# Performance work log

Measured on AMD Instinct MI355X. Metric: run time of the kernel, lower is better.

Reference implementation:

```python
import jax, jax.numpy as jnp
import numpy as np

S, T, D_OUT = 64, 256, 64
B = 64
HEADS = 2
D0 = S + T              # 320
D1 = D0 * (1 + HEADS)   # 960
D2 = D1 * (1 + HEADS)   # 2880
PARAM_SCALE = 0.02


def setup_inputs() -> dict:
    key = jax.random.key(0)
    k1, k2, k3, k4 = jax.random.split(key, 4)
    x = jax.random.normal(k1, (B, T, S), dtype=jnp.float32)
    A0 = jax.random.normal(k2, (HEADS, D0, D0), dtype=jnp.float32) * PARAM_SCALE
    A1 = jax.random.normal(k3, (HEADS, D1, D1), dtype=jnp.float32) * PARAM_SCALE
    Wo = jax.random.normal(k4, (D_OUT, D2), dtype=jnp.float32) * PARAM_SCALE
    return {"x": x, "A0": A0, "A1": A1, "Wo": Wo}


def _causal_self_attention(h, A):
    # h: [B, T, d], A: [H, d, d]
    Bsz, Tlen, d = h.shape
    H = A.shape[0]
    # bilinear scores per head: h @ A[i] @ h^T, vectorized over heads
    scores = jnp.einsum('btd,hde,bse->bhts', h, A, h)  # [B, H, T, T]
    neg_inf = jnp.asarray(float('-inf'), dtype=h.dtype)
    mask = jnp.triu(jnp.full((Tlen, Tlen), neg_inf, dtype=h.dtype), k=1)
    attn = jax.nn.softmax(scores + mask, axis=-1)
    out = jnp.einsum('bhts,bsd->bthd', attn, h)  # [B, T, H, d]
    return out.reshape(Bsz, Tlen, H * d)


def reference(x, A0, A1, Wo):
    Bsz, Tlen, _ = x.shape
    # one-hot positional encoding concatenated onto input
    pos = jnp.broadcast_to(jnp.eye(Tlen, dtype=x.dtype)[None], (Bsz, Tlen, Tlen))
    h = jnp.concatenate([x, pos], axis=-1)          # [B, T, S+T]
    h = jnp.concatenate([h, _causal_self_attention(h, A0)], axis=-1)  # [B, T, D1]
    h = jnp.concatenate([h, _causal_self_attention(h, A1)], axis=-1)  # [B, T, D2]
    logits = jnp.einsum('btd,od->bto', h, Wo)       # [B, T, d_out]
    return logits
```

## Files before the change

kernel.cpp:

```cpp
#include <hip/hip_runtime.h>
#include <math.h>

#define NB 64
#define NT 256
#define NS 64
#define ND0 320
#define ND1 960
#define ND2 2880
#define NH 2
#define DC 704
#define GP 1024

typedef __attribute__((ext_vector_type(8))) _Float16 f16x8;
typedef __attribute__((ext_vector_type(4))) float f32x4;
typedef __attribute__((ext_vector_type(4))) short short4v;

typedef const __attribute__((address_space(1))) void* gas_ptr;
typedef __attribute__((address_space(3))) void* las_ptr;
#define GLOAD16(g, l) __builtin_amdgcn_global_load_lds((gas_ptr)(g), (las_ptr)(l), 16, 0, 0)
#define MFMAH(a, b, c) __builtin_amdgcn_mfma_f32_16x16x32_f16((a), (b), (c), 0, 0, 0)

__device__ __forceinline__ short f2h(float v) {
    union { _Float16 h; short s; } u; u.h = (_Float16)v; return u.s;
}
__device__ __forceinline__ float h2f(short b) {
    union { _Float16 h; short s; } u; u.s = b; return (float)u.h;
}
__device__ __forceinline__ int swz(int o) { return o ^ (((o >> 7) & 7) << 4); }

template <int CMODE, int TERMS, bool AJUMP, bool SWZ>
__global__ __launch_bounds__(256, 3) void gemm128(
    const short* Ah, int lda, long sA,
    const short* Bh, const short* Bl, int ldb, long sB,
    float* Cf, int ldcf, long sCf,
    short* Chi, int ldch,
    const short* biasH, long ldbias,
    const float* biasA1,
    long hsA, long hsC,
    int gx, int K)
{
    int bx, by;
    if (SWZ) {
        int wg = blockIdx.x;
        int q = gridDim.x >> 3;
        int sid = (wg & 7) * q + (wg >> 3);
        bx = sid % gx; by = sid / gx;
    } else { bx = blockIdx.x; by = blockIdx.y; }
    int m0 = by * 128, n0 = bx * 128;
    if (CMODE == 0 && n0 > m0 + 127) return;
    long zLo = blockIdx.z & 63, zHi = blockIdx.z >> 6;
    const short* pAh = Ah + zLo * sA + zHi * hsA;
    const short* pBh = Bh + zLo * sB;
    const short* pBl = (TERMS == 2) ? (Bl + zLo * sB) : nullptr;

    __shared__ short lds[8192 * (1 + TERMS)];
    short* LAh = lds;
    short* LBh = lds + 8192;
    short* LBl = lds + 16384;

    int tid = threadIdx.x;
    int lane = tid & 63, w = tid >> 6;
    int wr = w >> 1, wc = w & 1;

    const short* aSH[4]; const short* bSH[4]; const short* bSL[4];
    int aLo[4], bLo[4];
#pragma unroll
    for (int j = 0; j < 4; ++j) {
        int o = j * 4096 + tid * 16;
        int c = swz(o); int r = c >> 7, col = (c & 127) >> 1;
        aSH[j] = pAh + (long)(m0 + r) * lda + col;
        aLo[j] = o >> 1;
        bSH[j] = pBh + (long)(n0 + r) * ldb + col;
        if (TERMS == 2) bSL[j] = pBl + (long)(n0 + r) * ldb + col;
        bLo[j] = o >> 1;
    }

    int oa[4][2], ob[4][2];
#pragma unroll
    for (int mf = 0; mf < 4; ++mf)
#pragma unroll
        for (int kf = 0; kf < 2; ++kf) {
            int row = wr * 64 + mf * 16 + (lane & 15);
            oa[mf][kf] = swz(row * 128 + (kf * 32 + ((lane >> 4) << 3)) * 2) >> 1;
        }
#pragma unroll
    for (int nf = 0; nf < 4; ++nf)
#pragma unroll
        for (int kf = 0; kf < 2; ++kf) {
            int row = wc * 64 + nf * 16 + (lane & 15);
            ob[nf][kf] = swz(row * 128 + (kf * 32 + ((lane >> 4) << 3)) * 2) >> 1;
        }

    f32x4 acc[4][4] = {};

    for (int k0 = 0; k0 < K; k0 += 64) {
        int step = (AJUMP && k0 == 0) ? 320 : 64;
#pragma unroll
        for (int j = 0; j < 4; ++j) {
            GLOAD16(aSH[j], LAh + aLo[j]);
            aSH[j] += step;
            GLOAD16(bSH[j], LBh + bLo[j]);
            bSH[j] += 64;
            if (TERMS == 2) { GLOAD16(bSL[j], LBl + bLo[j]); bSL[j] += 64; }
        }
        __syncthreads();
#pragma unroll
        for (int kf = 0; kf < 2; ++kf) {
            f16x8 vbh[4], vbl[4];
#pragma unroll
            for (int nf = 0; nf < 4; ++nf) {
                vbh[nf] = *(const f16x8*)(LBh + ob[nf][kf]);
                if (TERMS == 2) vbl[nf] = *(const f16x8*)(LBl + ob[nf][kf]);
            }
#pragma unroll
            for (int mf = 0; mf < 4; ++mf) {
                f16x8 vah = *(const f16x8*)(LAh + oa[mf][kf]);
#pragma unroll
                for (int nf = 0; nf < 4; ++nf) {
                    acc[mf][nf] = MFMAH(vah, vbh[nf], acc[mf][nf]);
                    if (TERMS == 2) acc[mf][nf] = MFMAH(vah, vbl[nf], acc[mf][nf]);
                }
            }
        }
        __syncthreads();
    }

#pragma unroll
    for (int mf = 0; mf < 4; ++mf)
#pragma unroll
        for (int nf = 0; nf < 4; ++nf) {
            f32x4 v = acc[mf][nf];
            int col  = n0 + wc * 64 + nf * 16 + (lane & 15);
            int rowb = m0 + wr * 64 + mf * 16 + ((lane >> 4) << 2);
            if (CMODE == 0) {
#pragma unroll
                for (int r = 0; r < 4; ++r) {
                    long o = (zLo * 256 + rowb + r) * ldbias + 64 + col + zHi * hsA;
                    v[r] += h2f(biasH[o]);
                }
#pragma unroll
                for (int r = 0; r < 4; ++r)
                    Cf[zLo * sCf + zHi * hsC + (long)(rowb + r) * ldcf + col] = v[r];
            } else {
                int head = col >> 10, colh = col & 1023;
                if (colh < ND1) {
                    const float* bA = biasA1 + (long)head * 921600 + colh;
#pragma unroll
                    for (int r = 0; r < 4; ++r) {
                        int t = (rowb + r) & 255;
                        float f = v[r] + bA[(long)(64 + t) * 960];
                        Chi[(long)(rowb + r) * ldch + col] = f2h(f);
                    }
                }
            }
        }
}

template <int BMODE, int TERMS, bool KCAUSAL, bool ACC, bool OUTU, bool BJUMP>
__global__ __launch_bounds__(256) void gemm_mfma(
    const short* Ah, int lda, long sA,
    const short* Bh, const short* Bl, int ldb, long sB, long hsB,
    float* Cf, int ldcf, long sCf,
    short* Chi, short* Clo, int ldch, long sCh,
    const float* biasF, long ldbias, long hsBias,
    long hsA, long hsC,
    short* UThi,
    int K)
{
    int m0 = blockIdx.y * 128, n0 = blockIdx.x * 64;
    long zLo = blockIdx.z & 63, zHi = blockIdx.z >> 6;
    const short* pAh = Ah + zLo * sA + zHi * hsA;
    const short* pBh = Bh + zLo * sB + zHi * hsB;
    const short* pBl = (TERMS == 2) ? (Bl + zLo * sB + zHi * hsB) : nullptr;

    __shared__ short lds[8192 + TERMS * 4096];
    short* LAh = lds;
    short* LBh = lds + 8192;
    short* LBl = lds + 12288;

    int tid = threadIdx.x;
    int lane = tid & 63, w = tid >> 6;
    int wr = w >> 1, wc = w & 1;

    const short* aSH[4]; const short* bSH[2]; const short* bSL[2];
    int aLo[4], bLo[2];
#pragma unroll
    for (int j = 0; j < 4; ++j) {
        int o = j * 4096 + tid * 16;
        int c = swz(o); int r = c >> 7, col = (c & 127) >> 1;
        aSH[j] = pAh + (long)(m0 + r) * lda + col;
        aLo[j] = o >> 1;
    }
#pragma unroll
    for (int j = 0; j < 2; ++j) {
        int o = j * 4096 + tid * 16;
        int c = swz(o); int r = c >> 7, col = (c & 127) >> 1;
        bSH[j] = pBh + (long)(n0 + r) * ldb + col;
        if (TERMS == 2) bSL[j] = pBl + (long)(n0 + r) * ldb + col;
        bLo[j] = o >> 1;
    }

    int oa[4][2], ob[2][2];
#pragma unroll
    for (int mf = 0; mf < 4; ++mf)
#pragma unroll
        for (int kf = 0; kf < 2; ++kf) {
            int row = wr * 64 + mf * 16 + (lane & 15);
            oa[mf][kf] = swz(row * 128 + (kf * 32 + ((lane >> 4) << 3)) * 2) >> 1;
        }
#pragma unroll
    for (int nf = 0; nf < 2; ++nf)
#pragma unroll
        for (int kf = 0; kf < 2; ++kf) {
            int row = wc * 32 + nf * 16 + (lane & 15);
            ob[nf][kf] = swz(row * 128 + (kf * 32 + ((lane >> 4) << 3)) * 2) >> 1;
        }

    f32x4 acc[4][2] = {};
    int Klim = KCAUSAL ? (K < m0 + 128 ? K : m0 + 128) : K;

    for (int k0 = 0; k0 < Klim; k0 += 64) {
#pragma unroll
        for (int j = 0; j < 4; ++j) {
            GLOAD16(aSH[j], LAh + aLo[j]);
            aSH[j] += 64;
        }
        long bstep = (BJUMP && k0 == 192) ? (1048576L - 192L) : 64L;
#pragma unroll
        for (int j = 0; j < 2; ++j) {
            GLOAD16(bSH[j], LBh + bLo[j]);
            bSH[j] += bstep;
            if (TERMS == 2) { GLOAD16(bSL[j], LBl + bLo[j]); bSL[j] += bstep; }
        }
        __syncthreads();
#pragma unroll
        for (int kf = 0; kf < 2; ++kf) {
            f16x8 vbh[2], vbl[2];
#pragma unroll
            for (int nf = 0; nf < 2; ++nf) {
                vbh[nf] = *(const f16x8*)(LBh + ob[nf][kf]);
                if (TERMS == 2) vbl[nf] = *(const f16x8*)(LBl + ob[nf][kf]);
            }
#pragma unroll
            for (int mf = 0; mf < 4; ++mf) {
                f16x8 vah = *(const f16x8*)(LAh + oa[mf][kf]);
#pragma unroll
                for (int nf = 0; nf < 2; ++nf) {
                    acc[mf][nf] = MFMAH(vah, vbh[nf], acc[mf][nf]);
                    if (TERMS == 2) acc[mf][nf] = MFMAH(vah, vbl[nf], acc[mf][nf]);
                }
            }
        }
        __syncthreads();
    }

#pragma unroll
    for (int mf = 0; mf < 4; ++mf)
#pragma unroll
        for (int nf = 0; nf < 2; ++nf) {
            f32x4 v = acc[mf][nf];
            int col  = n0 + wc * 32 + nf * 16 + (lane & 15);
            int rowb = m0 + wr * 64 + mf * 16 + ((lane >> 4) << 2);
            if (BMODE == 1) {
#pragma unroll
                for (int r = 0; r < 4; ++r) {
                    int t = (rowb + r) & 255;
                    v[r] += biasF[zLo * hsBias + (long)(64 + t) * ldbias + col];
                }
            } else if (BMODE == 3) {
#pragma unroll
                for (int r = 0; r < 4; ++r) {
                    int t = (rowb + r) & 255;
                    v[r] += biasF[(long)(col - n0) * 2880 + (n0 >> 6) * 960 + 64 + t];
                }
            }
            if (OUTU) {
                if (n0 == 0) {
#pragma unroll
                    for (int r = 0; r < 4; ++r)
                        Cf[(long)(rowb + r) * ldcf + col] = v[r];
                } else {
                    int head = (n0 >> 6) - 1;
                    int o = col - n0;
                    short hs[4];
#pragma unroll
                    for (int r = 0; r < 4; ++r) hs[r] = f2h(v[r]);
                    short4v th = {hs[0], hs[1], hs[2], hs[3]};
                    *(short4v*)(UThi + head * 1048576L + (long)o * 16384 + rowb) = th;
                }
            } else if (ACC) {
#pragma unroll
                for (int r = 0; r < 4; ++r)
                    Cf[zLo * sCf + (long)(rowb + r) * ldcf + col] += v[r];
            } else if (Cf) {
#pragma unroll
                for (int r = 0; r < 4; ++r)
                    Cf[zLo * sCf + (long)(rowb + r) * ldcf + col] = v[r];
            } else {
#pragma unroll
                for (int r = 0; r < 4; ++r) {
                    float f = v[r];
                    short hi = f2h(f);
                    Chi[zHi * hsC + zLo * sCh + (long)(rowb + r) * ldch + col] = hi;
                    if (Clo)
                        Clo[zHi * hsC + zLo * sCh + (long)(rowb + r) * ldch + col] = f2h(f - h2f(hi));
                }
            }
        }
}

__global__ __launch_bounds__(256) void build_h_rows(const float* __restrict__ x,
                                                    short* __restrict__ hhi) {
    int idx = blockIdx.x * 256 + threadIdx.x;
    int bt = idx >> 6, c = idx & 63;
    hhi[(long)bt * DC + c] = f2h(x[(long)bt * NS + c]);
}

__global__ __launch_bounds__(256) void build_hT_x(const float* __restrict__ x,
                                                  short* __restrict__ hTh,
                                                  short* __restrict__ hTl) {
    __shared__ float tile[32][33];
    int c0 = blockIdx.x * 32, t0 = blockIdx.y * 32, b = blockIdx.z;
    int tx = threadIdx.x, ty = threadIdx.y;
    const float* xb = x + (long)b * NT * NS;
#pragma unroll
    for (int i = ty; i < 32; i += 8) tile[i][tx] = xb[(long)(t0 + i) * NS + c0 + tx];
    __syncthreads();
    long base = (long)b * (NS * 256);
#pragma unroll
    for (int i = ty; i < 32; i += 8) {
        float v = tile[tx][i];
        short hi = f2h(v);
        hTh[base + (long)(c0 + i) * 256 + t0 + tx] = hi;
        hTl[base + (long)(c0 + i) * 256 + t0 + tx] = f2h(v - h2f(hi));
    }
}

__global__ void build_At(const float* __restrict__ A,
                         short* __restrict__ hi, short* __restrict__ lo,
                         int dN, int dK, int srcLd, int shift, int dSrcN) {
    __shared__ float tile[32][33];
    int k0 = blockIdx.x * 32, n0 = blockIdx.y * 32;
    long hbase = (long)blockIdx.z * srcLd * srcLd;
    int tx = threadIdx.x, ty = threadIdx.y;
#pragma unroll
    for (int i = ty; i < 32; i += 8) {
        int k = k0 + i;
        int srck = (k < 64) ? k : k + shift;
        tile[i][tx] = (n0 + tx < dSrcN) ? A[hbase + (long)srck * srcLd + n0 + tx] : 0.f;
    }
    __syncthreads();
    long obase = (long)blockIdx.z * dN * dK;
#pragma unroll
    for (int i = ty; i < 32; i += 8) {
        float v = tile[tx][i];
        short h = f2h(v);
        hi[obase + (long)(n0 + i) * dK + k0 + tx] = h;
        if (lo) lo[obase + (long)(n0 + i) * dK + k0 + tx] = f2h(v - h2f(h));
    }
}

__global__ __launch_bounds__(256) void build_Wf(const float* __restrict__ Wo,
                                                short* __restrict__ hi) {
    int idx = blockIdx.x * 256 + threadIdx.x;
    if (idx >= 192 * DC) return;
    int r = idx / DC, kc = idx - r * DC;
    int o = r & 63, chunk = r >> 6;
    int srck = (kc < 64) ? kc : kc + 256;
    hi[idx] = f2h(Wo[(long)o * ND2 + chunk * 960 + srck]);
}

__global__ __launch_bounds__(256) void softmax_split(const float* S,
                                                     short* pHi, short* pLo,
                                                     int ldo, long hs) {
    int row  = blockIdx.x * 4 + (threadIdx.x >> 6);
    int t    = row & (NT - 1);
    int hrow = row & 16383;
    int head = row >> 14;
    int lane = threadIdx.x & 63;
    int s0   = lane << 2;
    const float* p = S + (long)row * NT;

    float4 v = *(const float4*)(p + s0);
    float vv[4] = {v.x, v.y, v.z, v.w};
    float mx = -INFINITY;
#pragma unroll
    for (int j = 0; j < 4; ++j)
        if (s0 + j <= t) mx = fmaxf(mx, vv[j]);
    for (int off = 32; off; off >>= 1) mx = fmaxf(mx, __shfl_down(mx, off));
    mx = __shfl(mx, 0);

    float e[4]; float sum = 0.f;
#pragma unroll
    for (int j = 0; j < 4; ++j) {
        e[j] = (s0 + j <= t) ? __expf(vv[j] - mx) : 0.f;
        sum += e[j];
    }
    for (int off = 32; off; off >>= 1) sum += __shfl_down(sum, off);
    sum = __shfl(sum, 0);
    float inv = 1.f / sum;

    short hsv[4], lsv[4];
#pragma unroll
    for (int j = 0; j < 4; ++j) {
        float f = e[j] * inv;
        hsv[j] = f2h(f);
        lsv[j] = f2h(f - h2f(hsv[j]));
    }
    short4v hv = {hsv[0], hsv[1], hsv[2], hsv[3]};
    *(short4v*)(pHi + (long)head * hs + (long)hrow * ldo + s0) = hv;
    if (pLo) {
        short4v lv = {lsv[0], lsv[1], lsv[2], lsv[3]};
        *(short4v*)(pLo + (long)head * hs + (long)hrow * ldo + s0) = lv;
    }
}

__global__ __launch_bounds__(256) void build_h0(const float* __restrict__ x,
                                                float* __restrict__ h) {
    int idx = blockIdx.x * 256 + threadIdx.x;
    int bt = idx / ND0;
    int c  = idx - bt * ND0;
    int t  = bt & (NT - 1);
    float v;
    if (c < NS) v = x[(long)bt * NS + c];
    else        v = ((c - NS) == t) ? 1.0f : 0.0f;
    h[(long)bt * ND2 + c] = v;
}

template <bool BT, bool CAUSAL>
__global__ __launch_bounds__(256) void gemm64(
    const float* __restrict__ A, int lda, long sA,
    const float* __restrict__ Bm, int ldb, long sB,
    float* __restrict__ C, int ldc, long sC, int K)
{
    int m0 = blockIdx.y * 64, n0 = blockIdx.x * 64;
    if (CAUSAL && n0 > m0 + 63) return;
    long z = blockIdx.z;
    A += z * sA; Bm += z * sB; C += z * sC;

    __shared__ float As[16][68];
    __shared__ float Bs[16][68];

    int tid = threadIdx.x;
    int tx = tid & 15, ty = tid >> 4;
    int rowA = tid >> 2, kA = (tid & 3) << 2;
    int kB = tid >> 4,  colB = (tid & 15) << 2;

    float acc[4][4] = {};

    for (int k0 = 0; k0 < K; k0 += 16) {
        float4 av = *(const float4*)(A + (long)(m0 + rowA) * lda + k0 + kA);
        As[kA + 0][rowA] = av.x; As[kA + 1][rowA] = av.y;
        As[kA + 2][rowA] = av.z; As[kA + 3][rowA] = av.w;
        if (BT) {
            float4 bv = *(const float4*)(Bm + (long)(n0 + rowA) * ldb + k0 + kA);
            Bs[kA + 0][rowA] = bv.x; Bs[kA + 1][rowA] = bv.y;
            Bs[kA + 2][rowA] = bv.z; Bs[kA + 3][rowA] = bv.w;
        } else {
            float4 bv = *(const float4*)(Bm + (long)(k0 + kB) * ldb + n0 + colB);
            *(float4*)(&Bs[kB][colB]) = bv;
        }
        __syncthreads();
#pragma unroll
        for (int kk = 0; kk < 16; ++kk) {
            float4 a4 = *(const float4*)(&As[kk][ty << 2]);
            float4 b4 = *(const float4*)(&Bs[kk][tx << 2]);
            float a[4] = {a4.x, a4.y, a4.z, a4.w};
            float b[4] = {b4.x, b4.y, b4.z, b4.w};
#pragma unroll
            for (int i = 0; i < 4; ++i)
#pragma unroll
                for (int j = 0; j < 4; ++j)
                    acc[i][j] += a[i] * b[j];
        }
        __syncthreads();
    }
#pragma unroll
    for (int i = 0; i < 4; ++i) {
        float4 v = {acc[i][0], acc[i][1], acc[i][2], acc[i][3]};
        *(float4*)(C + (long)(m0 + (ty << 2) + i) * ldc + n0 + (tx << 2)) = v;
    }
}

__global__ __launch_bounds__(256) void softmax_causal(float* __restrict__ P) {
    int row  = blockIdx.x * 4 + (threadIdx.x >> 6);
    int t    = row & (NT - 1);
    int lane = threadIdx.x & 63;
    int s0   = lane << 2;
    float* p = P + (long)row * NT;

    float4 v = *(const float4*)(p + s0);
    float vv[4] = {v.x, v.y, v.z, v.w};
    float mx = -INFINITY;
#pragma unroll
    for (int j = 0; j < 4; ++j)
        if (s0 + j <= t) mx = fmaxf(mx, vv[j]);
    for (int off = 32; off; off >>= 1) mx = fmaxf(mx, __shfl_down(mx, off));
    mx = __shfl(mx, 0);

    float e[4]; float sum = 0.f;
#pragma unroll
    for (int j = 0; j < 4; ++j) {
        e[j] = (s0 + j <= t) ? __expf(vv[j] - mx) : 0.f;
        sum += e[j];
    }
    for (int off = 32; off; off >>= 1) sum += __shfl_down(sum, off);
    sum = __shfl(sum, 0);
    float inv = 1.f / sum;
    float4 o = {e[0] * inv, e[1] * inv, e[2] * inv, e[3] * inv};
    *(float4*)(p + s0) = o;
}

extern "C" void kernel_launch(void* const* d_in, const int* in_sizes, int n_in,
                              void* d_out, int out_size, void* d_ws, size_t ws_size,
                              hipStream_t stream) {
    const float* x  = (const float*)d_in[0];
    const float* A0 = (const float*)d_in[1];
    const float* A1 = (const float*)d_in[2];
    const float* Wo = (const float*)d_in[3];
    float* out = (float*)d_out;

    if (ws_size >= 175120384UL) {
        char* wsb = (char*)d_ws;
        short* hc_hi = (short*)(wsb);
        short* G_hi  = (short*)(wsb + 46137344L);
        float* S     = (float*)(wsb + 113246208L);
        short* P     = (short*)(wsb + 146800640L);
        short* hT_hi = (short*)(wsb + 163577856L);
        short* hT_lo = (short*)(wsb + 165675008L);
        short* At_hi = (short*)(wsb + 167772160L);
        short* Wf_hi = (short*)(wsb + 170655744L);
        short* UT_hi = (short*)(wsb + 170926080L);

        build_h_rows<<<4096, 256, 0, stream>>>(x, hc_hi);
        build_hT_x<<<dim3(2, 8, 64), dim3(32, 8), 0, stream>>>(x, hT_hi, hT_lo);
        build_Wf<<<528, 256, 0, stream>>>(Wo, Wf_hi);

        build_At<<<dim3(2, 10, 2), dim3(32, 8), 0, stream>>>(A0, At_hi, nullptr, ND0, 64, ND0, 0, ND0);
        gemm_mfma<1, 1, false, false, false, false><<<dim3(5, 128, 2), 256, 0, stream>>>(
            hc_hi, DC, 0L,
            At_hi, nullptr, 64, 20480L, 0L,
            nullptr, 0, 0L, G_hi, nullptr, 640, 320L,
            A0, 320L, 102400L,
            0L, 0L,
            nullptr, 64);
        gemm128<0, 1, false, false><<<dim3(2, 2, 128), 256, 0, stream>>>(
            G_hi, 640, 163840L,
            hc_hi, nullptr, DC, 180224L,
            S, NT, 65536L,
            nullptr, 0,
            G_hi, 640L,
            nullptr,
            320L, 4194304L, 0, 64);
        softmax_split<<<8192, 256, 0, stream>>>(S, hc_hi + 128, nullptr, DC, 320L);
        gemm_mfma<0, 2, true, false, false, false><<<dim3(1, 2, 128), 256, 0, stream>>>(
            hc_hi + 128, DC, 180224L,
            hT_hi, hT_lo, 256, 16384L, 0L,
            nullptr, 0, 0L,
            hc_hi + 64, nullptr, DC, 180224L,
            nullptr, 0L, 0L,
            320L, 320L,
            nullptr, 256);

        gemm_mfma<3, 1, false, false, true, false><<<dim3(3, 128, 1), 256, 0, stream>>>(
            hc_hi, DC, 0L,
            Wf_hi, nullptr, DC, 0L, 0L,
            out, NS, 0L, nullptr, nullptr, 0, 0L,
            Wo, 0L, 0L,
            0L, 0L,
            UT_hi, DC);

        build_At<<<dim3(22, 32, 2), dim3(32, 8), 0, stream>>>(A1, At_hi, nullptr, GP, DC, ND1, 256, ND1);
        gemm128<1, 1, false, true><<<dim3(2048, 1, 1), 256, 0, stream>>>(
            hc_hi, DC, 0L,
            At_hi, nullptr, DC, 0L,
            nullptr, 0, 0L,
            G_hi, 2048,
            nullptr, 0L,
            A1,
            0L, 0L, 16, DC);
        gemm128<0, 1, true, false><<<dim3(2, 2, 128), 256, 0, stream>>>(
            G_hi, 2048, 524288L,
            hc_hi, nullptr, DC, 180224L,
            S, NT, 65536L,
            nullptr, 0,
            G_hi, 2048L,
            nullptr,
            1024L, 4194304L, 0, DC);
        softmax_split<<<8192, 256, 0, stream>>>(S, P, nullptr, 512, 256L);
        gemm_mfma<0, 1, false, true, false, true><<<dim3(1, 2, 64), 256, 0, stream>>>(
            P, 512, 131072L,
            UT_hi, nullptr, 16384, 256L, 0L,
            out, NS, 16384L, nullptr, nullptr, 0, 0L,
            nullptr, 0L, 0L,
            0L, 0L,
            nullptr, 512);
        return;
    }

    float* ws = (float*)d_ws;
    float* h  = ws;
    float* G  = ws + 47185920L;
    float* Pf = ws + 47185920L + 15728640L;

    build_h0<<<(NB * NT * ND0) / 256, 256, 0, stream>>>(x, h);

    for (int layer = 0; layer < 2; ++layer) {
        int d = layer ? ND1 : ND0;
        const float* Am = layer ? A1 : A0;
        for (int head = 0; head < NH; ++head) {
            const float* Ah = Am + (long)head * d * d;
            gemm64<false, false><<<dim3(d / 64, 256, 1), 256, 0, stream>>>(
                h, ND2, 0L, Ah, d, 0L, G, d, 0L, d);
            gemm64<true, true><<<dim3(4, 4, NB), 256, 0, stream>>>(
                G, d, (long)NT * d, h, ND2, (long)NT * ND2,
                Pf, NT, (long)NT * NT, d);
            softmax_causal<<<(NB * NT) / 4, 256, 0, stream>>>(Pf);
            gemm64<false, false><<<dim3(d / 64, 4, NB), 256, 0, stream>>>(
                Pf, NT, (long)NT * NT, h, ND2, (long)NT * ND2,
                h + (long)d * (1 + head), ND2, (long)NT * ND2, NT);
        }
    }
    gemm64<true, false><<<dim3(1, 256, 1), 256, 0, stream>>>(
        h, ND2, 0L, Wo, ND2, 0L, out, NS, 0L, ND2);
}
```

Baseline: 189.6 us.

## Fuse causal score GEMM with softmax into a single full-row kernel

Adds a score_sm kernel that computes a 128x256 score tile per block, so each block holds complete rows. The kernel adds the positional bias, applies the causal mask, and does a two-wave max and sum reduction through LDS, then writes fp16 probabilities directly. The separate fp32 score round trip through global memory and the standalone softmax kernels are removed for both layers. In exchange, each block holds a large accumulator with only one block per CU allowed. Only 256 blocks are launched, which may leave many CUs idle.

```diff
diff --git a/kernel.cpp b/kernel.cpp
--- a/kernel.cpp
+++ b/kernel.cpp
@@ -27,6 +27,186 @@
     union { _Float16 h; short s; } u; u.s = b; return (float)u.h;
 }
 __device__ __forceinline__ int swz(int o) { return o ^ (((o >> 7) & 7) << 4); }
+
+template <int LAYER>
+__global__ __launch_bounds__(256, 1) void score_sm(
+    const short* __restrict__ G, int ldg, long sG, long hsG,
+    const short* __restrict__ hc,
+    short* __restrict__ pOut, int ldo, long sO, long hsO,
+    int K)
+{
+    int by = blockIdx.y;
+    int m0 = by * 128;
+    long zLo = blockIdx.z & 63, zHi = blockIdx.z >> 6;
+    const short* pAh = G + zLo * sG + zHi * hsG;
+    const short* pBh = hc + zLo * 180224L;
+
+    __shared__ short lds[24576];
+    int tid = threadIdx.x;
+    int lane = tid & 63, w = tid >> 6;
+    int wr = w >> 1, wc = w & 1;
+    int q = lane >> 4, l15 = lane & 15;
+
+    const short* aS[4]; const short* bS[8];
+    int dLo[4];
+#pragma unroll
+    for (int j = 0; j < 4; ++j) {
+        int o = j * 4096 + tid * 16;
+        int c = swz(o); int r = c >> 7, col = (c & 127) >> 1;
+        dLo[j] = o >> 1;
+        aS[j] = pAh + (long)(m0 + r) * ldg + col;
+        bS[j] = pBh + (long)r * DC + col;
+        bS[j + 4] = pBh + (long)(128 + r) * DC + col;
+    }
+
+    int oa[4][2], ob[8][2];
+#pragma unroll
+    for (int mf = 0; mf < 4; ++mf)
+#pragma unroll
+        for (int kf = 0; kf < 2; ++kf) {
+            int row = wr * 64 + mf * 16 + l15;
+            oa[mf][kf] = swz(row * 128 + (kf * 32 + (q << 3)) * 2) >> 1;
+        }
+#pragma unroll
+    for (int nf = 0; nf < 8; ++nf)
+#pragma unroll
+        for (int kf = 0; kf < 2; ++kf) {
+            int s = wc * 128 + nf * 16 + l15;
+            int half = s >> 7, sr = s & 127;
+            ob[nf][kf] = half * 8192 + (swz(sr * 128 + (kf * 32 + (q << 3)) * 2) >> 1);
+        }
+
+    f32x4 acc[4][8] = {};
+
+    for (int k0 = 0; k0 < K; k0 += 64) {
+        int step = (LAYER == 1 && k0 == 0) ? 320 : 64;
+#pragma unroll
+        for (int j = 0; j < 4; ++j) {
+            GLOAD16(aS[j], lds + dLo[j]);
+            aS[j] += step;
+            GLOAD16(bS[j], lds + 8192 + dLo[j]);
+            bS[j] += 64;
+        }
+        if (by) {
+#pragma unroll
+            for (int j = 0; j < 4; ++j) {
+                GLOAD16(bS[j + 4], lds + 16384 + dLo[j]);
+                bS[j + 4] += 64;
+            }
+        }
+        __syncthreads();
+        if (by || wc == 0) {
+#pragma unroll
+            for (int kf = 0; kf < 2; ++kf) {
+                f16x8 vb[8];
+#pragma unroll
+                for (int nf = 0; nf < 8; ++nf)
+                    vb[nf] = *(const f16x8*)(lds + 8192 + ob[nf][kf]);
+#pragma unroll
+                for (int mf = 0; mf < 4; ++mf) {
+                    f16x8 va = *(const f16x8*)(lds + oa[mf][kf]);
+#pragma unroll
+                    for (int nf = 0; nf < 8; ++nf)
+                        acc[mf][nf] = MFMAH(va, vb[nf], acc[mf][nf]);
+                }
+            }
+        }
+        __syncthreads();
+    }
+
+    float* red = (float*)lds;
+
+#pragma unroll
+    for (int mf = 0; mf < 4; ++mf)
+#pragma unroll
+        for (int nf = 0; nf < 8; ++nf) {
+            int colb = wc * 128 + nf * 16 + l15;
+#pragma unroll
+            for (int rr = 0; rr < 4; ++rr) {
+                int t = m0 + wr * 64 + mf * 16 + q * 4 + rr;
+                if (colb <= t) {
+                    long o = (zLo * 256 + t) * (long)ldg + 64 + colb + zHi * hsG;
+                    acc[mf][nf][rr] += h2f(G[o]);
+                } else {
+                    acc[mf][nf][rr] = -1e30f;
+                }
+            }
+        }
+
+    float rmax[4][4];
+#pragma unroll
+    for (int mf = 0; mf < 4; ++mf)
+#pragma unroll
+        for (int rr = 0; rr < 4; ++rr) {
+            float m = -1e30f;
+#pragma unroll
+            for (int nf = 0; nf < 8; ++nf) m = fmaxf(m, acc[mf][nf][rr]);
+            m = fmaxf(m, __shfl_xor(m, 1));
+            m = fmaxf(m, __shfl_xor(m, 2));
+            m = fmaxf(m, __shfl_xor(m, 4));
+            m = fmaxf(m, __shfl_xor(m, 8));
+            rmax[mf][rr] = m;
+        }
+    if (l15 == 0) {
+#pragma unroll
+        for (int mf = 0; mf < 4; ++mf)
+#pragma unroll
+            for (int rr = 0; rr < 4; ++rr)
+                red[wc * 128 + wr * 64 + mf * 16 + q * 4 + rr] = rmax[mf][rr];
+    }
+    __syncthreads();
+
+    float fullm[4][4];
+#pragma unroll
+    for (int mf = 0; mf < 4; ++mf)
+#pragma unroll
+        for (int rr = 0; rr < 4; ++rr) {
+            int row = wr * 64 + mf * 16 + q * 4 + rr;
+            fullm[mf][rr] = fmaxf(red[row], red[128 + row]);
+        }
+
+#pragma unroll
+    for (int mf = 0; mf < 4; ++mf)
+#pragma unroll
+        for (int rr = 0; rr < 4; ++rr) {
+            float s = 0.f;
+#pragma unroll
+            for (int nf = 0; nf < 8; ++nf) {
+                float a = acc[mf][nf][rr];
+                float e = (a > -1e29f) ? __expf(a - fullm[mf][rr]) : 0.f;
+                acc[mf][nf][rr] = e;
+                s += e;
+            }
+            s += __shfl_xor(s, 1);
+            s += __shfl_xor(s, 2);
+            s += __shfl_xor(s, 4);
+            s += __shfl_xor(s, 8);
+            rmax[mf][rr] = s;
+        }
+    if (l15 == 0) {
+#pragma unroll
+        for (int mf = 0; mf < 4; ++mf)
+#pragma unroll
+            for (int rr = 0; rr < 4; ++rr)
+                red[256 + wc * 128 + wr * 64 + mf * 16 + q * 4 + rr] = rmax[mf][rr];
+    }
+    __syncthreads();
+
+#pragma unroll
+    for (int mf = 0; mf < 4; ++mf)
+#pragma unroll
+        for (int rr = 0; rr < 4; ++rr) {
+            int row = wr * 64 + mf * 16 + q * 4 + rr;
+            int t = m0 + row;
+            float inv = 1.f / (red[256 + row] + red[256 + 128 + row]);
+            long base = zLo * sO + zHi * hsO + (long)t * ldo;
+#pragma unroll
+            for (int nf = 0; nf < 8; ++nf) {
+                int colb = wc * 128 + nf * 16 + l15;
+                pOut[base + colb] = f2h(acc[mf][nf][rr] * inv);
+            }
+        }
+}
 
 template <int CMODE, int TERMS, bool AJUMP, bool SWZ>
 __global__ __launch_bounds__(256, 3) void gemm128(
@@ -47,7 +227,6 @@
         bx = sid % gx; by = sid / gx;
     } else { bx = blockIdx.x; by = blockIdx.y; }
     int m0 = by * 128, n0 = bx * 128;
-    if (CMODE == 0 && n0 > m0 + 127) return;
     long zLo = blockIdx.z & 63, zHi = blockIdx.z >> 6;
     const short* pAh = Ah + zLo * sA + zHi * hsA;
     const short* pBh = Bh + zLo * sB;
@@ -133,11 +312,6 @@
             int col  = n0 + wc * 64 + nf * 16 + (lane & 15);
             int rowb = m0 + wr * 64 + mf * 16 + ((lane >> 4) << 2);
             if (CMODE == 0) {
-#pragma unroll
-                for (int r = 0; r < 4; ++r) {
-                    long o = (zLo * 256 + rowb + r) * ldbias + 64 + col + zHi * hsA;
-                    v[r] += h2f(biasH[o]);
-                }
 #pragma unroll
                 for (int r = 0; r < 4; ++r)
                     Cf[zLo * sCf + zHi * hsC + (long)(rowb + r) * ldcf + col] = v[r];
@@ -370,51 +544,6 @@
     hi[idx] = f2h(Wo[(long)o * ND2 + chunk * 960 + srck]);
 }
 
-__global__ __launch_bounds__(256) void softmax_split(const float* S,
-                                                     short* pHi, short* pLo,
-                                                     int ldo, long hs) {
-    int row  = blockIdx.x * 4 + (threadIdx.x >> 6);
-    int t    = row & (NT - 1);
-    int hrow = row & 16383;
-    int head = row >> 14;
-    int lane = threadIdx.x & 63;
-    int s0   = lane << 2;
-    const float* p = S + (long)row * NT;
-
-    float4 v = *(const float4*)(p + s0);
-    float vv[4] = {v.x, v.y, v.z, v.w};
-    float mx = -INFINITY;
-#pragma unroll
-    for (int j = 0; j < 4; ++j)
-        if (s0 + j <= t) mx = fmaxf(mx, vv[j]);
-    for (int off = 32; off; off >>= 1) mx = fmaxf(mx, __shfl_down(mx, off));
-    mx = __shfl(mx, 0);
-
-    float e[4]; float sum = 0.f;
-#pragma unroll
-    for (int j = 0; j < 4; ++j) {
-        e[j] = (s0 + j <= t) ? __expf(vv[j] - mx) : 0.f;
-        sum += e[j];
-    }
-    for (int off = 32; off; off >>= 1) sum += __shfl_down(sum, off);
-    sum = __shfl(sum, 0);
-    float inv = 1.f / sum;
-
-    short hsv[4], lsv[4];
-#pragma unroll
-    for (int j = 0; j < 4; ++j) {
-        float f = e[j] * inv;
-        hsv[j] = f2h(f);
-        lsv[j] = f2h(f - h2f(hsv[j]));
-    }
-    short4v hv = {hsv[0], hsv[1], hsv[2], hsv[3]};
-    *(short4v*)(pHi + (long)head * hs + (long)hrow * ldo + s0) = hv;
-    if (pLo) {
-        short4v lv = {lsv[0], lsv[1], lsv[2], lsv[3]};
-        *(short4v*)(pLo + (long)head * hs + (long)hrow * ldo + s0) = lv;
-    }
-}
-
 __global__ __launch_bounds__(256) void build_h0(const float* __restrict__ x,
                                                 float* __restrict__ h) {
     int idx = blockIdx.x * 256 + threadIdx.x;
@@ -524,7 +653,6 @@
         char* wsb = (char*)d_ws;
         short* hc_hi = (short*)(wsb);
         short* G_hi  = (short*)(wsb + 46137344L);
-        float* S     = (float*)(wsb + 113246208L);
         short* P     = (short*)(wsb + 146800640L);
         short* hT_hi = (short*)(wsb + 163577856L);
         short* hT_lo = (short*)(wsb + 165675008L);
@@ -544,15 +672,11 @@
             A0, 320L, 102400L,
             0L, 0L,
             nullptr, 64);
-        gemm128<0, 1, false, false><<<dim3(2, 2, 128), 256, 0, stream>>>(
-            G_hi, 640, 163840L,
-            hc_hi, nullptr, DC, 180224L,
-            S, NT, 65536L,
-            nullptr, 0,
-            G_hi, 640L,
-            nullptr,
-            320L, 4194304L, 0, 64);
-        softmax_split<<<8192, 256, 0, stream>>>(S, hc_hi + 128, nullptr, DC, 320L);
+        score_sm<0><<<dim3(1, 2, 128), 256, 0, stream>>>(
+            G_hi, 640, 163840L, 320L,
+            hc_hi,
+            hc_hi + 128, DC, 180224L, 320L,
+            64);
         gemm_mfma<0, 2, true, false, false, false><<<dim3(1, 2, 128), 256, 0, stream>>>(
             hc_hi + 128, DC, 180224L,
             hT_hi, hT_lo, 256, 16384L, 0L,
@@ -579,15 +703,11 @@
             nullptr, 0L,
             A1,
             0L, 0L, 16, DC);
-        gemm128<0, 1, true, false><<<dim3(2, 2, 128), 256, 0, stream>>>(
-            G_hi, 2048, 524288L,
-            hc_hi, nullptr, DC, 180224L,
-            S, NT, 65536L,
-            nullptr, 0,
-            G_hi, 2048L,
-            nullptr,
-            1024L, 4194304L, 0, DC);
-        softmax_split<<<8192, 256, 0, stream>>>(S, P, nullptr, 512, 256L);
+        score_sm<1><<<dim3(1, 2, 128), 256, 0, stream>>>(
+            G_hi, 2048, 524288L, 1024L,
+            hc_hi,
+            P, 512, 131072L, 256L,
+            DC);
         gemm_mfma<0, 1, false, true, false, true><<<dim3(1, 2, 64), 256, 0, stream>>>(
             P, 512, 131072L,
             UT_hi, nullptr, 16384, 256L, 0L,
```

Measured after the change: 226.5 us. 1.19x slower.

## Add dedicated 256x128 G1 GEMM with unpadded 1920 columns and drop lo-term split

Applied to the files above, without the earlier changes.

Replaces the generic swizzled gemm128 used for the layer-1 projection G = h·A1 with a dedicated gemmG1 kernel. The new kernel uses 256x128 tiles, fixed K=704 and an unpadded 1920-column output, where each head previously was padded to 1024 columns. It also removes the fp16 hi/lo error-compensation terms from the A·V GEMM over x (TERMS 2 to 1), and drops the lo outputs from the build and softmax kernels. This cuts redundant MFMA work, padded-column compute and extra memory writes, at the cost of reduced numerical precision in the first attention output.

```diff
diff --git a/kernel.cpp b/kernel.cpp
--- a/kernel.cpp
+++ b/kernel.cpp
@@ -9,7 +9,6 @@
 #define ND2 2880
 #define NH 2
 #define DC 704
-#define GP 1024
 
 typedef __attribute__((ext_vector_type(8))) _Float16 f16x8;
 typedef __attribute__((ext_vector_type(4))) float f32x4;
@@ -28,24 +27,110 @@
 }
 __device__ __forceinline__ int swz(int o) { return o ^ (((o >> 7) & 7) << 4); }
 
-template <int CMODE, int TERMS, bool AJUMP, bool SWZ>
+__global__ __launch_bounds__(256, 2) void gemmG1(
+    const short* __restrict__ hc,
+    const short* __restrict__ At,
+    short* __restrict__ G,
+    const float* __restrict__ A1)
+{
+    int wg = blockIdx.x;
+    int q8 = gridDim.x >> 3;
+    int sid = (wg & 7) * q8 + (wg >> 3);
+    int bx = sid % 15, by = sid / 15;
+    int m0 = by << 8, n0 = bx << 7;
+
+    __shared__ short lds[24576];
+    int tid = threadIdx.x;
+    int lane = tid & 63, w = tid >> 6;
+    int wm = w >> 1, wn = w & 1;
+    int q = lane >> 4, l15 = lane & 15;
+
+    const short* aS[8]; const short* bS[4];
+    int dA[8], dB[4];
+#pragma unroll
+    for (int j = 0; j < 8; ++j) {
+        int o = j * 4096 + tid * 16;
+        int c = swz(o); int r = c >> 7, col = (c & 127) >> 1;
+        aS[j] = hc + (long)(m0 + r) * DC + col;
+        dA[j] = o >> 1;
+    }
+#pragma unroll
+    for (int j = 0; j < 4; ++j) {
+        int o = j * 4096 + tid * 16;
+        int c = swz(o); int r = c >> 7, col = (c & 127) >> 1;
+        bS[j] = At + (long)(n0 + r) * DC + col;
+        dB[j] = o >> 1;
+    }
+
+    int oa[8][2], ob[4][2];
+#pragma unroll
+    for (int mf = 0; mf < 8; ++mf)
+#pragma unroll
+        for (int kf = 0; kf < 2; ++kf) {
+            int row = wm * 128 + mf * 16 + l15;
+            oa[mf][kf] = swz(row * 128 + (kf * 32 + (q << 3)) * 2) >> 1;
+        }
+#pragma unroll
+    for (int nf = 0; nf < 4; ++nf)
+#pragma unroll
+        for (int kf = 0; kf < 2; ++kf) {
+            int row = wn * 64 + nf * 16 + l15;
+            ob[nf][kf] = swz(row * 128 + (kf * 32 + (q << 3)) * 2) >> 1;
+        }
+
+    f32x4 acc[8][4] = {};
+
+    for (int k0 = 0; k0 < DC; k0 += 64) {
+#pragma unroll
+        for (int j = 0; j < 8; ++j) { GLOAD16(aS[j], lds + dA[j]); aS[j] += 64; }
+#pragma unroll
+        for (int j = 0; j < 4; ++j) { GLOAD16(bS[j], lds + 16384 + dB[j]); bS[j] += 64; }
+        __syncthreads();
+#pragma unroll
+        for (int kf = 0; kf < 2; ++kf) {
+            f16x8 vb[4];
+#pragma unroll
+            for (int nf = 0; nf < 4; ++nf)
+                vb[nf] = *(const f16x8*)(lds + 16384 + ob[nf][kf]);
+#pragma unroll
+            for (int mf = 0; mf < 8; ++mf) {
+                f16x8 va = *(const f16x8*)(lds + oa[mf][kf]);
+#pragma unroll
+                for (int nf = 0; nf < 4; ++nf)
+                    acc[mf][nf] = MFMAH(va, vb[nf], acc[mf][nf]);
+            }
+        }
+        __syncthreads();
+    }
+
+#pragma unroll
+    for (int mf = 0; mf < 8; ++mf)
+#pragma unroll
+        for (int nf = 0; nf < 4; ++nf) {
+            int col = n0 + wn * 64 + nf * 16 + l15;
+            int head = (col >= 960) ? 1 : 0;
+            int colh = col - head * 960;
+            const float* bA = A1 + (long)head * 921600 + colh;
+            int rowb = m0 + wm * 128 + mf * 16 + (q << 2);
+#pragma unroll
+            for (int r = 0; r < 4; ++r) {
+                int t = (rowb + r) & 255;
+                float f = acc[mf][nf][r] + bA[(long)(64 + t) * 960];
+                G[(long)(rowb + r) * 1920 + col] = f2h(f);
+            }
+        }
+}
+
+template <int CMODE, int TERMS, bool AJUMP>
 __global__ __launch_bounds__(256, 3) void gemm128(
     const short* Ah, int lda, long sA,
     const short* Bh, const short* Bl, int ldb, long sB,
     float* Cf, int ldcf, long sCf,
-    short* Chi, int ldch,
     const short* biasH, long ldbias,
-    const float* biasA1,
     long hsA, long hsC,
-    int gx, int K)
+    int K)
 {
-    int bx, by;
-    if (SWZ) {
-        int wg = blockIdx.x;
-        int q = gridDim.x >> 3;
-        int sid = (wg & 7) * q + (wg >> 3);
-        bx = sid % gx; by = sid / gx;
-    } else { bx = blockIdx.x; by = blockIdx.y; }
+    int bx = blockIdx.x, by = blockIdx.y;
     int m0 = by * 128, n0 = bx * 128;
     if (CMODE == 0 && n0 > m0 + 127) return;
     long zLo = blockIdx.z & 63, zHi = blockIdx.z >> 6;
@@ -132,27 +217,14 @@
             f32x4 v = acc[mf][nf];
             int col  = n0 + wc * 64 + nf * 16 + (lane & 15);
             int rowb = m0 + wr * 64 + mf * 16 + ((lane >> 4) << 2);
-            if (CMODE == 0) {
-#pragma unroll
-                for (int r = 0; r < 4; ++r) {
-                    long o = (zLo * 256 + rowb + r) * ldbias + 64 + col + zHi * hsA;
-                    v[r] += h2f(biasH[o]);
-                }
-#pragma unroll
-                for (int r = 0; r < 4; ++r)
-                    Cf[zLo * sCf + zHi * hsC + (long)(rowb + r) * ldcf + col] = v[r];
-            } else {
-                int head = col >> 10, colh = col & 1023;
-                if (colh < ND1) {
-                    const float* bA = biasA1 + (long)head * 921600 + colh;
-#pragma unroll
-                    for (int r = 0; r < 4; ++r) {
-                        int t = (rowb + r) & 255;
-                        float f = v[r] + bA[(long)(64 + t) * 960];
-                        Chi[(long)(rowb + r) * ldch + col] = f2h(f);
-                    }
-                }
-            }
+#pragma unroll
+            for (int r = 0; r < 4; ++r) {
+                long o = (zLo * 256 + rowb + r) * ldbias + 64 + col + zHi * hsA;
+                v[r] += h2f(biasH[o]);
+            }
+#pragma unroll
+            for (int r = 0; r < 4; ++r)
+                Cf[zLo * sCf + zHi * hsC + (long)(rowb + r) * ldcf + col] = v[r];
         }
 }
 
@@ -317,8 +389,7 @@
 }
 
 __global__ __launch_bounds__(256) void build_hT_x(const float* __restrict__ x,
-                                                  short* __restrict__ hTh,
-                                                  short* __restrict__ hTl) {
+                                                  short* __restrict__ hTh) {
     __shared__ float tile[32][33];
     int c0 = blockIdx.x * 32, t0 = blockIdx.y * 32, b = blockIdx.z;
     int tx = threadIdx.x, ty = threadIdx.y;
@@ -328,16 +399,12 @@
     __syncthreads();
     long base = (long)b * (NS * 256);
 #pragma unroll
-    for (int i = ty; i < 32; i += 8) {
-        float v = tile[tx][i];
-        short hi = f2h(v);
-        hTh[base + (long)(c0 + i) * 256 + t0 + tx] = hi;
-        hTl[base + (long)(c0 + i) * 256 + t0 + tx] = f2h(v - h2f(hi));
-    }
+    for (int i = ty; i < 32; i += 8)
+        hTh[base + (long)(c0 + i) * 256 + t0 + tx] = f2h(tile[tx][i]);
 }
 
 __global__ void build_At(const float* __restrict__ A,
-                         short* __restrict__ hi, short* __restrict__ lo,
+                         short* __restrict__ hi,
                          int dN, int dK, int srcLd, int shift, int dSrcN) {
     __shared__ float tile[32][33];
     int k0 = blockIdx.x * 32, n0 = blockIdx.y * 32;
@@ -352,12 +419,8 @@
     __syncthreads();
     long obase = (long)blockIdx.z * dN * dK;
 #pragma unroll
-    for (int i = ty; i < 32; i += 8) {
-        float v = tile[tx][i];
-        short h = f2h(v);
-        hi[obase + (long)(n0 + i) * dK + k0 + tx] = h;
-        if (lo) lo[obase + (long)(n0 + i) * dK + k0 + tx] = f2h(v - h2f(h));
-    }
+    for (int i = ty; i < 32; i += 8)
+        hi[obase + (long)(n0 + i) * dK + k0 + tx] = f2h(tile[tx][i]);
 }
 
 __global__ __launch_bounds__(256) void build_Wf(const float* __restrict__ Wo,
@@ -371,7 +434,7 @@
 }
 
 __global__ __launch_bounds__(256) void softmax_split(const float* S,
-                                                     short* pHi, short* pLo,
+                                                     short* pHi,
                                                      int ldo, long hs) {
     int row  = blockIdx.x * 4 + (threadIdx.x >> 6);
     int t    = row & (NT - 1);
@@ -400,19 +463,11 @@
     sum = __shfl(sum, 0);
     float inv = 1.f / sum;
 
-    short hsv[4], lsv[4];
-#pragma unroll
-    for (int j = 0; j < 4; ++j) {
-        float f = e[j] * inv;
-        hsv[j] = f2h(f);
-        lsv[j] = f2h(f - h2f(hsv[j]));
-    }
+    short hsv[4];
+#pragma unroll
+    for (int j = 0; j < 4; ++j) hsv[j] = f2h(e[j] * inv);
     short4v hv = {hsv[0], hsv[1], hsv[2], hsv[3]};
     *(short4v*)(pHi + (long)head * hs + (long)hrow * ldo + s0) = hv;
-    if (pLo) {
-        short4v lv = {lsv[0], lsv[1], lsv[2], lsv[3]};
-        *(short4v*)(pLo + (long)head * hs + (long)hrow * ldo + s0) = lv;
-    }
 }
 
 __global__ __launch_bounds__(256) void build_h0(const float* __restrict__ x,
@@ -527,16 +582,15 @@
         float* S     = (float*)(wsb + 113246208L);
         short* P     = (short*)(wsb + 146800640L);
         short* hT_hi = (short*)(wsb + 163577856L);
-        short* hT_lo = (short*)(wsb + 165675008L);
         short* At_hi = (short*)(wsb + 167772160L);
         short* Wf_hi = (short*)(wsb + 170655744L);
         short* UT_hi = (short*)(wsb + 170926080L);
 
         build_h_rows<<<4096, 256, 0, stream>>>(x, hc_hi);
-        build_hT_x<<<dim3(2, 8, 64), dim3(32, 8), 0, stream>>>(x, hT_hi, hT_lo);
+        build_hT_x<<<dim3(2, 8, 64), dim3(32, 8), 0, stream>>>(x, hT_hi);
         build_Wf<<<528, 256, 0, stream>>>(Wo, Wf_hi);
 
-        build_At<<<dim3(2, 10, 2), dim3(32, 8), 0, stream>>>(A0, At_hi, nullptr, ND0, 64, ND0, 0, ND0);
+        build_At<<<dim3(2, 10, 2), dim3(32, 8), 0, stream>>>(A0, At_hi, ND0, 64, ND0, 0, ND0);
         gemm_mfma<1, 1, false, false, false, false><<<dim3(5, 128, 2), 256, 0, stream>>>(
             hc_hi, DC, 0L,
             At_hi, nullptr, 64, 20480L, 0L,
@@ -544,18 +598,16 @@
             A0, 320L, 102400L,
             0L, 0L,
             nullptr, 64);
-        gemm128<0, 1, false, false><<<dim3(2, 2, 128), 256, 0, stream>>>(
+        gemm128<0, 1, false><<<dim3(2, 2, 128), 256, 0, stream>>>(
             G_hi, 640, 163840L,
             hc_hi, nullptr, DC, 180224L,
             S, NT, 65536L,
-            nullptr, 0,
             G_hi, 640L,
-            nullptr,
-            320L, 4194304L, 0, 64);
-        softmax_split<<<8192, 256, 0, stream>>>(S, hc_hi + 128, nullptr, DC, 320L);
-        gemm_mfma<0, 2, true, false, false, false><<<dim3(1, 2, 128), 256, 0, stream>>>(
+            320L, 4194304L, 64);
+        softmax_split<<<8192, 256, 0, stream>>>(S, hc_hi + 128, DC, 320L);
+        gemm_mfma<0, 1, true, false, false, false><<<dim3(1, 2, 128), 256, 0, stream>>>(
             hc_hi + 128, DC, 180224L,
-            hT_hi, hT_lo, 256, 16384L, 0L,
+            hT_hi, nullptr, 256, 16384L, 0L,
             nullptr, 0, 0L,
             hc_hi + 64, nullptr, DC, 180224L,
             nullptr, 0L, 0L,
@@ -570,24 +622,15 @@
             0L, 0L,
             UT_hi, DC);
 
-        build_At<<<dim3(22, 32, 2), dim3(32, 8), 0, stream>>>(A1, At_hi, nullptr, GP, DC, ND1, 256, ND1);
-        gemm128<1, 1, false, true><<<dim3(2048, 1, 1), 256, 0, stream>>>(
-            hc_hi, DC, 0L,
-            At_hi, nullptr, DC, 0L,
-            nullptr, 0, 0L,
-            G_hi, 2048,
-            nullptr, 0L,
-            A1,
-            0L, 0L, 16, DC);
-        gemm128<0, 1, true, false><<<dim3(2, 2, 128), 256, 0, stream>>>(
-            G_hi, 2048, 524288L,
+        build_At<<<dim3(22, 30, 2), dim3(32, 8), 0, stream>>>(A1, At_hi, 960, DC, ND1, 256, ND1);
+        gemmG1<<<960, 256, 0, stream>>>(hc_hi, At_hi, G_hi, A1);
+        gemm128<0, 1, true><<<dim3(2, 2, 128), 256, 0, stream>>>(
+            G_hi, 1920, 491520L,
             hc_hi, nullptr, DC, 180224L,
             S, NT, 65536L,
-            nullptr, 0,
-            G_hi, 2048L,
-            nullptr,
-            1024L, 4194304L, 0, DC);
-        softmax_split<<<8192, 256, 0, stream>>>(S, P, nullptr, 512, 256L);
+            G_hi, 1920L,
+            960L, 4194304L, DC);
+        softmax_split<<<8192, 256, 0, stream>>>(S, P, 512, 256L);
         gemm_mfma<0, 1, false, true, false, true><<<dim3(1, 2, 64), 256, 0, stream>>>(
             P, 512, 131072L,
             UT_hi, nullptr, 16384, 256L, 0L,
```

Result: faster. 177.5 us (-6.4%).
